# Kernel optimization log

Hardware: AMD Instinct MI355X
Metric: run time of the kernel (lower is better)

Reference implementation:

```python
import jax, jax.numpy as jnp
import numpy as np

E = 65536          # number of edges (cell pairs)
D = 256            # hidden_dim
P = 8              # n_lr_pairs


def setup_inputs() -> dict:
    key = jax.random.key(0)
    k1, k2, k3, k4, k5, k6, k7 = jax.random.split(key, 7)
    scale = 1.0 / np.sqrt(D)
    z_src = jax.random.normal(k1, (E, D), dtype=jnp.float32)
    z_dst = jax.random.normal(k2, (E, D), dtype=jnp.float32)
    lr_pair_idx = jax.random.randint(k3, (E,), 0, P, dtype=jnp.int64)
    # Per-LR-pair Linear(D, D): y = x @ W.T + b  (torch convention, W: [out, in])
    W_lr = jax.random.normal(k4, (P, D, D), dtype=jnp.float32) * scale
    b_lr = jax.random.normal(k5, (P, D), dtype=jnp.float32) * scale
    # nn.Bilinear(D, D, 1): weight [1, D, D], bias [1]
    W_bil = jax.random.normal(k6, (1, D, D), dtype=jnp.float32) * scale
    b_bil = jax.random.normal(k7, (1,), dtype=jnp.float32) * scale
    return {"z_src": z_src, "z_dst": z_dst, "W_lr": W_lr, "b_lr": b_lr,
            "W_bil": W_bil, "b_bil": b_bil, "lr_pair_idx": lr_pair_idx}


def _forward(z_src, z_dst, W_lr, b_lr, W_bil, b_bil, lr_pair_idx):
    # Per-LR-pair linear projection of z_src (MoE-style routing).
    # Fixed small loop over P experts; each iteration is a dense GEMM over
    # all E edges, masked to the edges routed to that pair. All idx values
    # lie in [0, P), so the zeros-init in the original is fully overwritten.
    z_proj = jnp.zeros_like(z_src)
    for p in range(P):
        mask = (lr_pair_idx == p)[:, None]                      # [E, 1]
        y_p = z_src @ W_lr[p].T + b_lr[p]                       # [E, D]
        z_proj = jnp.where(mask, y_p, z_proj)
    # Bilinear scoring: score_e = z_proj_e @ W_bil[0] @ z_dst_e + b_bil
    t = z_proj @ W_bil[0]                                       # [E, D]
    scores = jnp.sum(t * z_dst, axis=-1, keepdims=True) + b_bil  # [E, 1]
    return scores


def reference(z_src, z_dst, W_lr, b_lr, W_bil, b_bil, lr_pair_idx):
    return _forward(z_src, z_dst, W_lr, b_lr, W_bil, b_bil, lr_pair_idx)
```

## Files before the change

kernel.cpp:

```cpp
#include <hip/hip_runtime.h>
#include <hip/hip_bf16.h>
#include <cstddef>

#define NE 65536
#define ND 256
#define NP 8
#define RBLK 64
#define EPB (NE / RBLK)
#define MAXT 1032

typedef short bf16x8 __attribute__((ext_vector_type(8)));
typedef float f32x4  __attribute__((ext_vector_type(4)));

__device__ __forceinline__ unsigned short f2bf(float f) {
  unsigned int u = __float_as_uint(f);
  u += 0x7FFFu + ((u >> 16) & 1u);
  return (unsigned short)(u >> 16);
}
__device__ __forceinline__ float bf2f(unsigned short h) {
  return __uint_as_float(((unsigned int)h) << 16);
}

__device__ __forceinline__ int sniff_is32(const void* idxraw, int* lflag) {
  int tid = threadIdx.x;
  if (tid == 0) *lflag = 0;
  __syncthreads();
  const unsigned int* w = (const unsigned int*)idxraw;
  unsigned int val = w[((blockIdx.x & 63) * 256 + (tid & 255)) * 2 + 1];
  if (__any(val != 0) && (tid & 63) == 0) atomicOr(lflag, 1);
  __syncthreads();
  return *lflag;
}
__device__ __forceinline__ int load_idx(const void* idxraw, int is32, int e) {
  return is32 ? ((const int*)idxraw)[e] : (int)((const long long*)idxraw)[e];
}

__global__ __launch_bounds__(256) void k_hist(const void* __restrict__ idxraw,
                                              int* __restrict__ counts) {
  __shared__ int h[NP];
  __shared__ int lflag;
  int tid = threadIdx.x;
  int is32 = sniff_is32(idxraw, &lflag);
  if (tid < NP) h[tid] = 0;
  __syncthreads();
  int base = blockIdx.x * EPB;
#pragma unroll
  for (int i = 0; i < EPB / 256; ++i) {
    int p = load_idx(idxraw, is32, base + tid + i * 256);
    atomicAdd(&h[p], 1);
  }
  __syncthreads();
  if (tid < NP) counts[blockIdx.x * NP + tid] = h[tid];
}

__global__ __launch_bounds__(64) void k_scan(const int* __restrict__ counts,
                                             int* __restrict__ hdr,
                                             int* __restrict__ bases) {
  __shared__ int cnt[NP];
  __shared__ int off[NP + 1];
  int q = threadIdx.x;
  if (q < NP) {
    int s = 0;
    for (int b = 0; b < RBLK; ++b) s += counts[b * NP + q];
    cnt[q] = s;
  }
  __syncthreads();
  if (q == 0) {
    int o = 0, tt = 0;
    for (int p = 0; p < NP; ++p) {
      off[p] = o; hdr[p] = o; hdr[9 + p] = tt;
      o += cnt[p];
      tt += (cnt[p] + 63) >> 6;
    }
    off[NP] = o; hdr[NP] = o; hdr[9 + NP] = tt;
  }
  __syncthreads();
  if (q < NP) {
    int run = off[q];
    for (int b = 0; b < RBLK; ++b) {
      bases[b * NP + q] = run;
      run += counts[b * NP + q];
    }
  }
}

__global__ __launch_bounds__(256) void k_scatter(const void* __restrict__ idxraw,
                                                 const int* __restrict__ bases,
                                                 int* __restrict__ perm) {
  __shared__ int cur[NP];
  __shared__ int lflag;
  int tid = threadIdx.x;
  int is32 = sniff_is32(idxraw, &lflag);
  if (tid < NP) cur[tid] = bases[blockIdx.x * NP + tid];
  __syncthreads();
  int base = blockIdx.x * EPB;
#pragma unroll
  for (int i = 0; i < EPB / 256; ++i) {
    int e = base + tid + i * 256;
    int p = load_idx(idxraw, is32, e);
    int slot = atomicAdd(&cur[p], 1);
    perm[slot] = e;
  }
}

__global__ __launch_bounds__(256) void k_prep(const float* __restrict__ Wbil,
                                              const float* __restrict__ blr,
                                              unsigned short* __restrict__ WbT,
                                              float* __restrict__ v) {
  int b = blockIdx.x, t = threadIdx.x;
  if (b < 32) {
    int s = b * 256 + t;
    int kt = s >> 10, c = (s >> 6) & 15, l = s & 63;
    int col = c * 16 + (l & 15);
    int k0 = kt * 32 + (l >> 4) * 8;
    union { uint4 u; unsigned short h[8]; } uu;
#pragma unroll
    for (int j = 0; j < 8; ++j)
      uu.h[j] = f2bf(Wbil[(k0 + j) * ND + col]);
    *(uint4*)(WbT + (size_t)s * 8) = uu.u;
  } else {
    int p = b - 32;
    float s = 0.f;
    for (int k = 0; k < ND; ++k)
      s = fmaf(blr[p * ND + k], Wbil[k * ND + t], s);
    v[p * ND + t] = s;
  }
}

__global__ __launch_bounds__(256) void k_cpre(const float* __restrict__ Wlr,
                                              const unsigned short* __restrict__ WbT,
                                              unsigned short* __restrict__ Cst) {
  __shared__ unsigned short aF[2048 * 8];
  int blk = blockIdx.x;
  int p = blk >> 2;
  int i0 = (blk & 3) * 64;
  int tid = threadIdx.x;
  const float* Wp = Wlr + (size_t)p * ND * ND;
#pragma unroll
  for (int it = 0; it < 8; ++it) {
    int s = tid + it * 256;
    int kt = s >> 8, r = (s >> 6) & 3, l = s & 63;
    int i = r * 16 + (l & 15);
    int k0 = kt * 32 + (l >> 4) * 8;
    union { uint4 u; unsigned short h[8]; } uu;
#pragma unroll
    for (int j = 0; j < 8; ++j)
      uu.h[j] = f2bf(Wp[(size_t)(k0 + j) * ND + i0 + i]);
    *(uint4*)(aF + (size_t)s * 8) = uu.u;
  }
  __syncthreads();
  int w = tid >> 6, l = tid & 63;
  f32x4 zero = {0.f, 0.f, 0.f, 0.f};
  f32x4 acc[16];
#pragma unroll
  for (int c = 0; c < 16; ++c) acc[c] = zero;
  for (int kt = 0; kt < 8; ++kt) {
    bf16x8 a = *(const bf16x8*)(aF + (size_t)((kt * 4 + w) * 64 + l) * 8);
#pragma unroll
    for (int c = 0; c < 16; ++c) {
      bf16x8 bb = *(const bf16x8*)(WbT + (size_t)((kt * 16 + c) * 64 + l) * 8);
      acc[c] = __builtin_amdgcn_mfma_f32_16x16x32_bf16(a, bb, acc[c], 0, 0, 0);
    }
  }
  unsigned short* Cp = Cst + (size_t)p * ND * ND;
#pragma unroll
  for (int c = 0; c < 16; ++c) {
#pragma unroll
    for (int q = 0; q < 4; ++q) {
      int i = i0 + w * 16 + ((l >> 4) * 4) + q;
      int j = c * 16 + (l & 15);
      int pos = ((i >> 5) * 16 + (j >> 4)) * 512 + (((i >> 3) & 3) * 16 + (j & 15)) * 8 + (i & 7);
      Cp[pos] = f2bf(acc[c][q]);
    }
  }
}

__global__ __launch_bounds__(512, 4) void k_main(const float* __restrict__ zsrc,
                                                 const float* __restrict__ zdst,
                                                 const int* __restrict__ perm,
                                                 const int* __restrict__ hdr,
                                                 const unsigned short* __restrict__ Cst,
                                                 const float* __restrict__ v,
                                                 const float* __restrict__ bbil,
                                                 float* __restrict__ out) {
  __shared__ unsigned short aF[16384];
  __shared__ unsigned short zL[16384];
  __shared__ float red[8][64];
  __shared__ int eids[64];
  __shared__ int shdr[18];
  int tid = threadIdx.x;
  if (tid < 18) shdr[tid] = hdr[tid];
  __syncthreads();
  int bid = blockIdx.x;
  if (bid >= shdr[9 + NP]) return;
  int p = 0;
  while (p < NP - 1 && bid >= shdr[9 + p + 1]) ++p;
  int t = bid - shdr[9 + p];
  int cnt = shdr[p + 1] - shdr[p];
  int ebase = shdr[p] + t * 64;
  int nrow = cnt - t * 64; if (nrow > 64) nrow = 64;
  if (tid < 64) eids[tid] = perm[ebase + (tid < nrow ? tid : nrow - 1)];
  __syncthreads();
  int w = tid >> 6, l = tid & 63;

  int kt0 = l >> 3, pos0 = (l & 7) >> 1, par0 = l & 1;
#pragma unroll
  for (int i = 0; i < 8; ++i) {
    int row = w * 8 + i;
    int e = eids[row];
    float4 fs = *(const float4*)(zsrc + (size_t)e * ND + l * 4);
    float4 fd = *(const float4*)(zdst + (size_t)e * ND + l * 4);
    union { ushort4 u; unsigned short hh[4]; } us, ud;
    us.hh[0] = f2bf(fs.x); us.hh[1] = f2bf(fs.y); us.hh[2] = f2bf(fs.z); us.hh[3] = f2bf(fs.w);
    ud.hh[0] = f2bf(fd.x); ud.hh[1] = f2bf(fd.y); ud.hh[2] = f2bf(fd.z); ud.hh[3] = f2bf(fd.w);
    *(ushort4*)((char*)zL + row * 512 + ((l * 8) ^ ((row & 7) << 4))) = ud.u;
    unsigned byte = (unsigned)(((kt0 * 4 + (row >> 4)) << 10) | (pos0 << 8) | ((row & 15) << 4) | (par0 << 3));
    byte ^= (unsigned)(((kt0 & 3) << 5) ^ ((pos0 & 1) << 4));
    *(ushort4*)((char*)aF + byte) = us.u;
  }
  __syncthreads();

  const unsigned short* Cp = Cst + (size_t)p * ND * ND;
  f32x4 zero = {0.f, 0.f, 0.f, 0.f};
  f32x4 acc[4][2];
#pragma unroll
  for (int sr = 0; sr < 4; ++sr)
#pragma unroll
    for (int cl = 0; cl < 2; ++cl) acc[sr][cl] = zero;
  int pos = l >> 4;
#pragma unroll
  for (int kt = 0; kt < 8; ++kt) {
    bf16x8 a[4];
#pragma unroll
    for (int sr = 0; sr < 4; ++sr) {
      unsigned byte = (unsigned)(((kt * 4 + sr) << 10) | (pos << 8) | ((l & 15) << 4));
      byte ^= (unsigned)(((kt & 3) << 5) ^ ((pos & 1) << 4));
      a[sr] = *(const bf16x8*)((const char*)aF + byte);
    }
#pragma unroll
    for (int cl = 0; cl < 2; ++cl) {
      bf16x8 bb = *(const bf16x8*)(Cp + (size_t)((kt * 16 + (w * 2 + cl)) * 64 + l) * 8);
#pragma unroll
      for (int sr = 0; sr < 4; ++sr)
        acc[sr][cl] = __builtin_amdgcn_mfma_f32_16x16x32_bf16(a[sr], bb, acc[sr][cl], 0, 0, 0);
    }
  }

  float vloc[2];
#pragma unroll
  for (int cl = 0; cl < 2; ++cl)
    vloc[cl] = v[p * ND + (w * 2 + cl) * 16 + (l & 15)];
#pragma unroll
  for (int sr = 0; sr < 4; ++sr) {
#pragma unroll
    for (int q = 0; q < 4; ++q) {
      int row = sr * 16 + (l >> 4) * 4 + q;
      unsigned swz = (unsigned)((row & 7) << 4);
      float sv = 0.f;
#pragma unroll
      for (int cl = 0; cl < 2; ++cl) {
        int col = (w * 2 + cl) * 16 + (l & 15);
        unsigned zb = (unsigned)(row * 512) + (((unsigned)(col * 2)) ^ swz);
        sv = fmaf(acc[sr][cl][q] + vloc[cl], bf2f(*(const unsigned short*)((const char*)zL + zb)), sv);
      }
      sv += __shfl_xor(sv, 1, 64);
      sv += __shfl_xor(sv, 2, 64);
      sv += __shfl_xor(sv, 4, 64);
      sv += __shfl_xor(sv, 8, 64);
      if ((l & 15) == 0) red[w][row] = sv;
    }
  }
  __syncthreads();
  if (tid < 64 && tid < nrow) {
    float sc = bbil[0];
#pragma unroll
    for (int ww = 0; ww < 8; ++ww) sc += red[ww][tid];
    out[eids[tid]] = sc;
  }
}

extern "C" void kernel_launch(void* const* d_in, const int* in_sizes, int n_in,
                              void* d_out, int out_size, void* d_ws, size_t ws_size,
                              hipStream_t stream) {
  const float* zsrc = (const float*)d_in[0];
  const float* zdst = (const float*)d_in[1];
  const float* Wlr  = (const float*)d_in[2];
  const float* blr  = (const float*)d_in[3];
  const float* Wbil = (const float*)d_in[4];
  const float* bbil = (const float*)d_in[5];
  const void*  idx  = (const void*)d_in[6];
  float* out = (float*)d_out;

  char* ws = (char*)d_ws;
  int* hdr    = (int*)ws;
  int* counts = (int*)(ws + 4096);
  int* bases  = (int*)(ws + 8192);
  int* perm   = (int*)(ws + 16384);
  unsigned short* WbT = (unsigned short*)(ws + 16384 + (size_t)NE * 4);
  float* v = (float*)(ws + 16384 + (size_t)NE * 4 + 131072);
  unsigned short* Cst = (unsigned short*)(ws + 16384 + (size_t)NE * 4 + 131072 + 8192);

  k_prep<<<40, 256, 0, stream>>>(Wbil, blr, WbT, v);
  k_hist<<<RBLK, 256, 0, stream>>>(idx, counts);
  k_scan<<<1, 64, 0, stream>>>(counts, hdr, bases);
  k_scatter<<<RBLK, 256, 0, stream>>>(idx, bases, perm);
  k_cpre<<<32, 256, 0, stream>>>(Wlr, WbT, Cst);
  k_main<<<MAXT, 512, 0, stream>>>(zsrc, zdst, perm, hdr, Cst, v, bbil, out);
}
```

Measured before the change: 84.50 us.

## Stage gathered fp32 rows directly into LDS and halve rows per tile

The gather of z_src/z_dst rows now uses direct global-to-LDS loads into fp32 shared buffers with an XOR swizzle. The bf16 conversion of the A operand moves into the MFMA loop, and z_dst is read in fp32 during the epilogue. The tile drops from 64 to 32 edges per block, doubling the block count so the same LDS budget still fits. This aims to cut register staging and raise occupancy and latency hiding, at the cost of repeated in-loop conversion and more re-reads of the weight matrix C across blocks.

```diff
diff --git a/kernel.cpp b/kernel.cpp
--- a/kernel.cpp
+++ b/kernel.cpp
@@ -7,18 +7,18 @@
 #define NP 8
 #define RBLK 64
 #define EPB (NE / RBLK)
-#define MAXT 1032
+#define TR 32
+#define MAXT 2056
 
 typedef short bf16x8 __attribute__((ext_vector_type(8)));
 typedef float f32x4  __attribute__((ext_vector_type(4)));
+typedef const __attribute__((address_space(1))) unsigned int* gas_t;
+typedef __attribute__((address_space(3))) unsigned int* las_t;
 
 __device__ __forceinline__ unsigned short f2bf(float f) {
   unsigned int u = __float_as_uint(f);
   u += 0x7FFFu + ((u >> 16) & 1u);
   return (unsigned short)(u >> 16);
-}
-__device__ __forceinline__ float bf2f(unsigned short h) {
-  return __uint_as_float(((unsigned int)h) << 16);
 }
 
 __device__ __forceinline__ int sniff_is32(const void* idxraw, int* lflag) {
@@ -70,7 +70,7 @@
     for (int p = 0; p < NP; ++p) {
       off[p] = o; hdr[p] = o; hdr[9 + p] = tt;
       o += cnt[p];
-      tt += (cnt[p] + 63) >> 6;
+      tt += (cnt[p] + TR - 1) / TR;
     }
     off[NP] = o; hdr[NP] = o; hdr[9 + NP] = tt;
   }
@@ -183,10 +183,10 @@
                                                  const float* __restrict__ v,
                                                  const float* __restrict__ bbil,
                                                  float* __restrict__ out) {
-  __shared__ unsigned short aF[16384];
-  __shared__ unsigned short zL[16384];
-  __shared__ float red[8][64];
-  __shared__ int eids[64];
+  __shared__ float zsF[TR * 256];
+  __shared__ float zdF[TR * 256];
+  __shared__ float red[8][TR];
+  __shared__ int eids[TR];
   __shared__ int shdr[18];
   int tid = threadIdx.x;
   if (tid < 18) shdr[tid] = hdr[tid];
@@ -197,51 +197,55 @@
   while (p < NP - 1 && bid >= shdr[9 + p + 1]) ++p;
   int t = bid - shdr[9 + p];
   int cnt = shdr[p + 1] - shdr[p];
-  int ebase = shdr[p] + t * 64;
-  int nrow = cnt - t * 64; if (nrow > 64) nrow = 64;
-  if (tid < 64) eids[tid] = perm[ebase + (tid < nrow ? tid : nrow - 1)];
+  int ebase = shdr[p] + t * TR;
+  int nrow = cnt - t * TR; if (nrow > TR) nrow = TR;
+  if (tid < TR) eids[tid] = perm[ebase + (tid < nrow ? tid : nrow - 1)];
   __syncthreads();
   int w = tid >> 6, l = tid & 63;
 
-  int kt0 = l >> 3, pos0 = (l & 7) >> 1, par0 = l & 1;
-#pragma unroll
-  for (int i = 0; i < 8; ++i) {
-    int row = w * 8 + i;
+#pragma unroll
+  for (int i = 0; i < 4; ++i) {
+    int row = w * 4 + i;
     int e = eids[row];
-    float4 fs = *(const float4*)(zsrc + (size_t)e * ND + l * 4);
-    float4 fd = *(const float4*)(zdst + (size_t)e * ND + l * 4);
-    union { ushort4 u; unsigned short hh[4]; } us, ud;
-    us.hh[0] = f2bf(fs.x); us.hh[1] = f2bf(fs.y); us.hh[2] = f2bf(fs.z); us.hh[3] = f2bf(fs.w);
-    ud.hh[0] = f2bf(fd.x); ud.hh[1] = f2bf(fd.y); ud.hh[2] = f2bf(fd.z); ud.hh[3] = f2bf(fd.w);
-    *(ushort4*)((char*)zL + row * 512 + ((l * 8) ^ ((row & 7) << 4))) = ud.u;
-    unsigned byte = (unsigned)(((kt0 * 4 + (row >> 4)) << 10) | (pos0 << 8) | ((row & 15) << 4) | (par0 << 3));
-    byte ^= (unsigned)(((kt0 & 3) << 5) ^ ((pos0 & 1) << 4));
-    *(ushort4*)((char*)aF + byte) = us.u;
+    int s = row & 3;
+    unsigned srcoff = ((((unsigned)(l >> 1) ^ (unsigned)s) << 5) | ((unsigned)(l & 1) << 4));
+    const float* gs = zsrc + (size_t)e * ND + (srcoff >> 2);
+    const float* gd = zdst + (size_t)e * ND + (srcoff >> 2);
+    __builtin_amdgcn_global_load_lds((gas_t)(const void*)gs,
+                                     (las_t)(void*)((char*)zsF + row * 1024), 16, 0, 0);
+    __builtin_amdgcn_global_load_lds((gas_t)(const void*)gd,
+                                     (las_t)(void*)((char*)zdF + row * 1024), 16, 0, 0);
   }
   __syncthreads();
 
   const unsigned short* Cp = Cst + (size_t)p * ND * ND;
   f32x4 zero = {0.f, 0.f, 0.f, 0.f};
-  f32x4 acc[4][2];
-#pragma unroll
-  for (int sr = 0; sr < 4; ++sr)
+  f32x4 acc[2][2];
+#pragma unroll
+  for (int sr = 0; sr < 2; ++sr)
 #pragma unroll
     for (int cl = 0; cl < 2; ++cl) acc[sr][cl] = zero;
-  int pos = l >> 4;
+  int hh = l >> 4, rr = l & 15;
 #pragma unroll
   for (int kt = 0; kt < 8; ++kt) {
-    bf16x8 a[4];
-#pragma unroll
-    for (int sr = 0; sr < 4; ++sr) {
-      unsigned byte = (unsigned)(((kt * 4 + sr) << 10) | (pos << 8) | ((l & 15) << 4));
-      byte ^= (unsigned)(((kt & 3) << 5) ^ ((pos & 1) << 4));
-      a[sr] = *(const bf16x8*)((const char*)aF + byte);
+    bf16x8 a[2];
+#pragma unroll
+    for (int sr = 0; sr < 2; ++sr) {
+      int row = sr * 16 + rr;
+      unsigned pidx = (unsigned)((kt * 4 + hh) ^ (row & 3));
+      const char* bp = (const char*)zsF + row * 1024 + (pidx << 5);
+      float4 f0 = *(const float4*)(bp);
+      float4 f1 = *(const float4*)(bp + 16);
+      union { bf16x8 vv; unsigned short h[8]; } ua;
+      ua.h[0] = f2bf(f0.x); ua.h[1] = f2bf(f0.y); ua.h[2] = f2bf(f0.z); ua.h[3] = f2bf(f0.w);
+      ua.h[4] = f2bf(f1.x); ua.h[5] = f2bf(f1.y); ua.h[6] = f2bf(f1.z); ua.h[7] = f2bf(f1.w);
+      a[sr] = ua.vv;
     }
 #pragma unroll
     for (int cl = 0; cl < 2; ++cl) {
       bf16x8 bb = *(const bf16x8*)(Cp + (size_t)((kt * 16 + (w * 2 + cl)) * 64 + l) * 8);
 #pragma unroll
-      for (int sr = 0; sr < 4; ++sr)
+      for (int sr = 0; sr < 2; ++sr)
         acc[sr][cl] = __builtin_amdgcn_mfma_f32_16x16x32_bf16(a[sr], bb, acc[sr][cl], 0, 0, 0);
     }
   }
@@ -249,29 +253,30 @@
   float vloc[2];
 #pragma unroll
   for (int cl = 0; cl < 2; ++cl)
-    vloc[cl] = v[p * ND + (w * 2 + cl) * 16 + (l & 15)];
-#pragma unroll
-  for (int sr = 0; sr < 4; ++sr) {
+    vloc[cl] = v[p * ND + (w * 2 + cl) * 16 + rr];
+#pragma unroll
+  for (int sr = 0; sr < 2; ++sr) {
 #pragma unroll
     for (int q = 0; q < 4; ++q) {
-      int row = sr * 16 + (l >> 4) * 4 + q;
-      unsigned swz = (unsigned)((row & 7) << 4);
+      int row = sr * 16 + hh * 4 + q;
+      int s = row & 3;
       float sv = 0.f;
 #pragma unroll
       for (int cl = 0; cl < 2; ++cl) {
-        int col = (w * 2 + cl) * 16 + (l & 15);
-        unsigned zb = (unsigned)(row * 512) + (((unsigned)(col * 2)) ^ swz);
-        sv = fmaf(acc[sr][cl][q] + vloc[cl], bf2f(*(const unsigned short*)((const char*)zL + zb)), sv);
+        int col = (w * 2 + cl) * 16 + rr;
+        unsigned byte = (unsigned)(row * 1024) + ((((unsigned)(col >> 3) ^ (unsigned)s) << 5) | ((unsigned)(col & 7) << 2));
+        float zv = *(const float*)((const char*)zdF + byte);
+        sv = fmaf(acc[sr][cl][q] + vloc[cl], zv, sv);
       }
       sv += __shfl_xor(sv, 1, 64);
       sv += __shfl_xor(sv, 2, 64);
       sv += __shfl_xor(sv, 4, 64);
       sv += __shfl_xor(sv, 8, 64);
-      if ((l & 15) == 0) red[w][row] = sv;
-    }
-  }
-  __syncthreads();
-  if (tid < 64 && tid < nrow) {
+      if (rr == 0) red[w][row] = sv;
+    }
+  }
+  __syncthreads();
+  if (tid < TR && tid < nrow) {
     float sc = bbil[0];
 #pragma unroll
     for (int ww = 0; ww < 8; ++ww) sc += red[ww][tid];
```

After: 92.21 us. +9.1%, slower.
